# Performance work log

Hardware: AMD Instinct MI355X
Metric: run time of the kernel (lower is better)

## Reference

```python
import jax, jax.numpy as jnp
import numpy as np

N = 50000   # nodes
E = 800000  # edges (avg degree 16)
D = 128     # input feature dim
H = 128     # hidden dim
C = 10      # num classes
G = 16      # graphs in batch


def setup_inputs() -> dict:
    key = jax.random.key(0)
    ks = jax.random.split(key, 12)
    def w(k, shape):
        return jax.random.normal(k, shape, jnp.float32) / np.sqrt(shape[0]).astype(np.float32)
    return {
        "h": jax.random.normal(ks[0], (N, D), jnp.float32),
        "src": jax.random.randint(ks[1], (E,), 0, N, jnp.int32),
        "dst": jax.random.randint(ks[2], (E,), 0, N, jnp.int32),
        "graph_ids": jnp.sort(jax.random.randint(ks[3], (N,), 0, G, jnp.int32)),
        "W1a": w(ks[4], (D, H)), "b1a": jnp.zeros((H,), jnp.float32),
        "W2a": w(ks[5], (H, H)), "b2a": jnp.zeros((H,), jnp.float32),
        "W1b": w(ks[6], (H, H)), "b1b": jnp.zeros((H,), jnp.float32),
        "W2b": w(ks[7], (H, H)), "b2b": jnp.zeros((H,), jnp.float32),
        "Wc1": w(ks[8], (H, H)), "bc1": jnp.zeros((H,), jnp.float32),
        "Wc2": w(ks[9], (H, C)), "bc2": jnp.zeros((C,), jnp.float32),
    }


def _gin_layer(h, src, dst, W1, b1, W2, b2):
    # GIN aggregation, eps=0: z_i = h_i + sum_{j in N(i)} h_j
    agg = jax.ops.segment_sum(h[src], dst, num_segments=N)
    z = h + agg
    # 2-layer MLP apply function with relu activation ('relu' arg of GINLayer)
    z = jax.nn.relu(z @ W1 + b1)
    return jax.nn.relu(z @ W2 + b2)


def reference(h, src, dst, graph_ids, W1a, b1a, W2a, b2a,
              W1b, b1b, W2b, b2b, Wc1, bc1, Wc2, bc2):
    h = _gin_layer(h, src, dst, W1a, b1a, W2a, b2a)   # [N, H]
    h = _gin_layer(h, src, dst, W1b, b1b, W2b, b2b)   # [N, H]
    # dgl.mean_nodes over the batched graph
    sums = jax.ops.segment_sum(h, graph_ids, num_segments=G)                # [G, H]
    cnts = jax.ops.segment_sum(jnp.ones((N, 1), h.dtype), graph_ids, num_segments=G)
    h_g = sums / jnp.maximum(cnts, 1.0)
    # cls MLP: linear -> relu -> linear (logits)
    out = jax.nn.relu(h_g @ Wc1 + bc1) @ Wc2 + bc2    # [G, C]
    return out
```

## Files before the change

### kernel.cpp

```cpp
#include <hip/hip_runtime.h>
#include <stdint.h>

#define NN 50000
#define EE 800000
#define DD 128
#define GG 16
#define CC 10
#define NBK 196
#define BCH 4096
#define SMAX 5120
#define FT (NBK * NBK)
#define NSCN ((FT + 255) / 256)

typedef unsigned short u16;
typedef __bf16 bf16x8 __attribute__((ext_vector_type(8)));
typedef float f32x4 __attribute__((ext_vector_type(4)));
typedef unsigned int u32x4 __attribute__((ext_vector_type(4)));
typedef float fl4 __attribute__((ext_vector_type(4)));

__device__ inline u16 f2bf(float f) {
    unsigned u = __float_as_uint(f);
    u = u + 0x7fffu + ((u >> 16) & 1u);
    return (u16)(u >> 16);
}
__device__ inline unsigned pack2(float a, float b) {
    return (unsigned)f2bf(a) | ((unsigned)f2bf(b) << 16);
}
__device__ inline float bf2f(unsigned bits16) { return __uint_as_float(bits16 << 16); }
__device__ inline void acc8(float* a, uint4 v) {
    a[0] += __uint_as_float(v.x << 16); a[1] += __uint_as_float(v.x & 0xffff0000u);
    a[2] += __uint_as_float(v.y << 16); a[3] += __uint_as_float(v.y & 0xffff0000u);
    a[4] += __uint_as_float(v.z << 16); a[5] += __uint_as_float(v.z & 0xffff0000u);
    a[6] += __uint_as_float(v.w << 16); a[7] += __uint_as_float(v.w & 0xffff0000u);
}
__device__ inline void mand(uint4& v, int p) {
    unsigned m = p ? 0xffffffffu : 0u;
    v.x &= m; v.y &= m; v.z &= m; v.w &= m;
}
__device__ inline void nt_store16(void* p, uint4 v) {
    u32x4 x; x.x = v.x; x.y = v.y; x.z = v.z; x.w = v.w;
    __builtin_nontemporal_store(x, (u32x4*)p);
}
__device__ inline uint4 nt_load16(const void* p) {
    u32x4 x = __builtin_nontemporal_load((const u32x4*)p);
    uint4 r; r.x = x.x; r.y = x.y; r.z = x.z; r.w = x.w;
    return r;
}
__device__ inline float4 nt_loadf4(const float* p) {
    fl4 x = __builtin_nontemporal_load((const fl4*)p);
    float4 r; r.x = x.x; r.y = x.y; r.z = x.z; r.w = x.w;
    return r;
}

#define PZ (GG * DD)
#define PC (NN * DD / 4)
#define PW (4 * DD * DD)
#define PTOT (PZ + PC + PW)
#define PBLK ((PTOT + 255) / 256)

__global__ __launch_bounds__(256) void prepsort_kernel(
    const float* __restrict__ h,
    const float* __restrict__ a, const float* __restrict__ b,
    const float* __restrict__ c, const float* __restrict__ d,
    int* __restrict__ zbase, u16* __restrict__ H0, u16* __restrict__ wt,
    const int* __restrict__ dst, int* __restrict__ counts) {
    __shared__ int hist[NBK];
    int blk = blockIdx.x, t = threadIdx.x;
    if (blk < NBK) {
        for (int i = t; i < NBK; i += 256) hist[i] = 0;
        __syncthreads();
        int e0 = blk * BCH, e1 = min(e0 + BCH, EE);
        for (int e = e0 + t; e < e1; e += 256) atomicAdd(&hist[dst[e] >> 8], 1);
        __syncthreads();
        for (int i = t; i < NBK; i += 256) counts[i * NBK + blk] = hist[i];
        return;
    }
    int i = (blk - NBK) * 256 + t;
    if (i < PZ) { zbase[i] = 0; return; }
    i -= PZ;
    if (i < PC) {
        int j = i * 4;
        float4 v = nt_loadf4(h + j);
        ushort4 o;
        o.x = f2bf(v.x); o.y = f2bf(v.y); o.z = f2bf(v.z); o.w = f2bf(v.w);
        *(ushort4*)(H0 + j) = o;
        return;
    }
    i -= PC;
    if (i < PW) {
        int m = i >> 14, r = i & 16383, k = r >> 7, j = r & 127;
        const float* W = (m == 0) ? a : (m == 1) ? b : (m == 2) ? c : d;
        wt[(m << 14) + (j << 7) + k] = f2bf(W[(k << 7) + j]);
    }
}

__global__ __launch_bounds__(256) void scanA_kernel(int* __restrict__ counts,
                                                    int* __restrict__ bsum) {
    __shared__ int tmp[256];
    int t = threadIdx.x, idx = blockIdx.x * 256 + t;
    int v = (idx < FT) ? counts[idx] : 0;
    tmp[t] = v; __syncthreads();
    for (int off = 1; off < 256; off <<= 1) {
        int x = (t >= off) ? tmp[t - off] : 0;
        __syncthreads();
        tmp[t] += x;
        __syncthreads();
    }
    if (idx < FT) counts[idx] = tmp[t] - v;
    if (t == 255) bsum[blockIdx.x] = tmp[255];
}

__global__ __launch_bounds__(256) void scanB_kernel(int* __restrict__ bsum,
                                                    const int* __restrict__ gids,
                                                    int* __restrict__ gstart) {
    __shared__ int tmp[256];
    int t = threadIdx.x;
    if (t <= GG) {
        int lo = 0, hi = NN;
        while (lo < hi) { int mid = (lo + hi) >> 1; if (gids[mid] < t) lo = mid + 1; else hi = mid; }
        gstart[t] = lo;
    }
    int v = (t < NSCN) ? bsum[t] : 0;
    tmp[t] = v; __syncthreads();
    for (int off = 1; off < 256; off <<= 1) {
        int x = (t >= off) ? tmp[t - off] : 0;
        __syncthreads();
        tmp[t] += x;
        __syncthreads();
    }
    if (t < NSCN) bsum[t] = tmp[t] - v;
}

__global__ __launch_bounds__(256) void scanC_kernel(int* __restrict__ counts,
                                                    const int* __restrict__ bsum) {
    int idx = blockIdx.x * 256 + threadIdx.x;
    if (idx < FT) counts[idx] += bsum[blockIdx.x];
}

__global__ __launch_bounds__(256) void sortP3_kernel(const int* __restrict__ src,
                                                     const int* __restrict__ dst,
                                                     const int* __restrict__ counts,
                                                     int* __restrict__ epack) {
    __shared__ int lhist[NBK + 1];
    __shared__ int lcur[NBK];
    __shared__ int goff[NBK];
    __shared__ int tmp[256];
    __shared__ int sbuf[BCH];
    int b = blockIdx.x, t = threadIdx.x;
    int e0 = b * BCH, e1 = min(e0 + BCH, EE), n = e1 - e0;

    for (int i = t; i < NBK; i += 256) lhist[i] = 0;
    __syncthreads();
    for (int e = e0 + t; e < e1; e += 256) atomicAdd(&lhist[dst[e] >> 8], 1);
    __syncthreads();
    int v = (t < NBK) ? lhist[t] : 0;
    tmp[t] = v; __syncthreads();
    for (int off = 1; off < 256; off <<= 1) {
        int x = (t >= off) ? tmp[t - off] : 0;
        __syncthreads();
        tmp[t] += x;
        __syncthreads();
    }
    if (t < NBK) {
        int excl = tmp[t] - v;
        lcur[t] = excl;
        lhist[t] = excl;
        goff[t] = counts[t * NBK + b] - excl;
    }
    if (t == 0) lhist[NBK] = n;
    __syncthreads();
    for (int e = e0 + t; e < e1; e += 256) {
        int dd = dst[e], s = src[e];
        int p = atomicAdd(&lcur[dd >> 8], 1);
        sbuf[p] = (s << 8) | (dd & 255);
    }
    __syncthreads();
    for (int i = t; i < n; i += 256) {
        int pk = sbuf[i];
        int lo = 0, hi = NBK - 1;
        while (lo < hi) { int mid = (lo + hi + 1) >> 1; if (lhist[mid] <= i) lo = mid; else hi = mid - 1; }
        epack[goff[lo] + i] = pk;
    }
}

__global__ __launch_bounds__(256) void sortP4_kernel(const int* __restrict__ epack,
                                                     const int* __restrict__ counts,
                                                     int* __restrict__ offs,
                                                     int* __restrict__ ssrc) {
    __shared__ int hist[256];
    __shared__ int curs[256];
    __shared__ int stage[SMAX];
    int j = blockIdx.x, t = threadIdx.x;
    int n0 = j << 8;
    int b0 = counts[j * NBK];
    int b1 = (j < NBK - 1) ? counts[(j + 1) * NBK] : EE;
    hist[t] = 0;
    __syncthreads();
    for (int e = b0 + t; e < b1; e += 256) atomicAdd(&hist[epack[e] & 255], 1);
    __syncthreads();
    int deg = hist[t];
    for (int off = 1; off < 256; off <<= 1) {
        int x = (t >= off) ? hist[t - off] : 0;
        __syncthreads();
        hist[t] += x;
        __syncthreads();
    }
    int loff = hist[t] - deg;
    curs[t] = loff;
    if (n0 + t <= NN) offs[n0 + t] = b0 + loff;
    __syncthreads();
    for (int e = b0 + t; e < b1; e += 256) {
        int pk = epack[e];
        int p = atomicAdd(&curs[pk & 255], 1);
        stage[p] = pk >> 8;
    }
    __syncthreads();
    int n = b1 - b0;
    for (int i = t; i < n; i += 256) ssrc[b0 + i] = stage[i];
}

__global__ __launch_bounds__(256) void agg_kernel(
    const u16* __restrict__ Hin, const int* __restrict__ offs,
    const int* __restrict__ ssrc, u16* __restrict__ Z) {
    int gid = blockIdx.x * 32 + (threadIdx.x >> 3);
    int lid = threadIdx.x & 7;
    if (gid >= 2 * NN) return;
    int node = gid >> 1;
    int foff = (gid & 1) * 64 + lid * 8;
    const u16* base = Hin + foff;

    float acc[8] = {0.f, 0.f, 0.f, 0.f, 0.f, 0.f, 0.f, 0.f};
    uint4 vs = *(const uint4*)(base + (size_t)node * DD);
    int e0 = offs[node], e1 = offs[node + 1];
    acc8(acc, vs);

    int nch = (e1 - e0 + 7) >> 3;
    if (nch > 0) {
        int elast = e1 - 1;
        int i0 = ssrc[e0];
        int i1 = ssrc[min(e0 + 1, elast)];
        int i2 = ssrc[min(e0 + 2, elast)];
        int i3 = ssrc[min(e0 + 3, elast)];
        int i4 = ssrc[min(e0 + 4, elast)];
        int i5 = ssrc[min(e0 + 5, elast)];
        int i6 = ssrc[min(e0 + 6, elast)];
        int i7 = ssrc[min(e0 + 7, elast)];
        int eb = e0;
        for (int c = 0; c < nch; c++) {
            int ebn = eb + 8;
            int n0 = i0, n1 = i1, n2 = i2, n3 = i3, n4 = i4, n5 = i5, n6 = i6, n7 = i7;
            if (c + 1 < nch) {
                n0 = ssrc[ebn];
                n1 = ssrc[min(ebn + 1, elast)];
                n2 = ssrc[min(ebn + 2, elast)];
                n3 = ssrc[min(ebn + 3, elast)];
                n4 = ssrc[min(ebn + 4, elast)];
                n5 = ssrc[min(ebn + 5, elast)];
                n6 = ssrc[min(ebn + 6, elast)];
                n7 = ssrc[min(ebn + 7, elast)];
            }
            uint4 v0 = *(const uint4*)(base + (size_t)i0 * DD);
            uint4 v1 = *(const uint4*)(base + (size_t)i1 * DD);
            uint4 v2 = *(const uint4*)(base + (size_t)i2 * DD);
            uint4 v3 = *(const uint4*)(base + (size_t)i3 * DD);
            uint4 v4 = *(const uint4*)(base + (size_t)i4 * DD);
            uint4 v5 = *(const uint4*)(base + (size_t)i5 * DD);
            uint4 v6 = *(const uint4*)(base + (size_t)i6 * DD);
            uint4 v7 = *(const uint4*)(base + (size_t)i7 * DD);
            mand(v1, eb + 1 < e1); mand(v2, eb + 2 < e1); mand(v3, eb + 3 < e1);
            mand(v4, eb + 4 < e1); mand(v5, eb + 5 < e1); mand(v6, eb + 6 < e1);
            mand(v7, eb + 7 < e1);
            acc8(acc, v0); acc8(acc, v1); acc8(acc, v2); acc8(acc, v3);
            acc8(acc, v4); acc8(acc, v5); acc8(acc, v6); acc8(acc, v7);
            i0 = n0; i1 = n1; i2 = n2; i3 = n3; i4 = n4; i5 = n5; i6 = n6; i7 = n7;
            eb = ebn;
        }
    }
    uint4 o;
    o.x = pack2(acc[0], acc[1]); o.y = pack2(acc[2], acc[3]);
    o.z = pack2(acc[4], acc[5]); o.w = pack2(acc[6], acc[7]);
    nt_store16(Z + (size_t)node * DD + foff, o);
}

__global__ __launch_bounds__(256) void mlp_kernel(
    const u16* __restrict__ Zin, const u16* __restrict__ Wt1, const float* __restrict__ b1,
    const u16* __restrict__ Wt2, const float* __restrict__ b2,
    u16* __restrict__ Hout, const int* __restrict__ gids, float* __restrict__ pool) {
    __shared__ u16 zb[64][136];
    __shared__ int garr[64];
    const int tid = threadIdx.x;
    const int wave = tid >> 6;
    const int lane = tid & 63;
    const int m16 = lane & 15;
    const int quad = lane >> 4;
    const int row0 = blockIdx.x * 64 + wave * 16;
    const int brow0 = blockIdx.x * 64;

    if (pool && tid < 64) garr[tid] = (brow0 + tid < NN) ? gids[brow0 + tid] : 0;

#pragma unroll
    for (int p = 0; p < 4; p++) {
        int idx = p * 64 + lane;
        int r = idx >> 4, ch = idx & 15;
        if (row0 + r < NN) {
            uint4 v = nt_load16(Zin + (size_t)(row0 + r) * DD + ch * 8);
            *(uint4*)&zb[wave * 16 + r][ch * 8] = v;
        }
    }

    bf16x8 afr[4];
#pragma unroll
    for (int kk = 0; kk < 4; kk++)
        afr[kk] = *(const bf16x8*)&zb[wave * 16 + m16][kk * 32 + quad * 8];
    f32x4 acc[8];
#pragma unroll
    for (int nt = 0; nt < 8; nt++) acc[nt] = (f32x4){0.f, 0.f, 0.f, 0.f};
#pragma unroll
    for (int kk = 0; kk < 4; kk++) {
#pragma unroll
        for (int nt = 0; nt < 8; nt++) {
            bf16x8 bfr = *(const bf16x8*)(Wt1 + ((nt * 16 + m16) << 7) + kk * 32 + quad * 8);
            acc[nt] = __builtin_amdgcn_mfma_f32_16x16x32_bf16(afr[kk], bfr, acc[nt], 0, 0, 0);
        }
    }
#pragma unroll
    for (int nt = 0; nt < 8; nt++) {
        int col = nt * 16 + m16;
        float bias = b1[col];
#pragma unroll
        for (int r = 0; r < 4; r++) {
            float yv = acc[nt][r] + bias;
            yv = yv > 0.f ? yv : 0.f;
            zb[wave * 16 + quad * 4 + r][col] = f2bf(yv);
        }
    }

#pragma unroll
    for (int kk = 0; kk < 4; kk++)
        afr[kk] = *(const bf16x8*)&zb[wave * 16 + m16][kk * 32 + quad * 8];
#pragma unroll
    for (int nt = 0; nt < 8; nt++) acc[nt] = (f32x4){0.f, 0.f, 0.f, 0.f};
#pragma unroll
    for (int kk = 0; kk < 4; kk++) {
#pragma unroll
        for (int nt = 0; nt < 8; nt++) {
            bf16x8 bfr = *(const bf16x8*)(Wt2 + ((nt * 16 + m16) << 7) + kk * 32 + quad * 8);
            acc[nt] = __builtin_amdgcn_mfma_f32_16x16x32_bf16(afr[kk], bfr, acc[nt], 0, 0, 0);
        }
    }
#pragma unroll
    for (int nt = 0; nt < 8; nt++) {
        int col = nt * 16 + m16;
        float bias = b2[col];
#pragma unroll
        for (int r = 0; r < 4; r++) {
            float ov = acc[nt][r] + bias;
            ov = ov > 0.f ? ov : 0.f;
            zb[wave * 16 + quad * 4 + r][col] = f2bf(ov);
        }
    }
#pragma unroll
    for (int p = 0; p < 4; p++) {
        int idx = p * 64 + lane;
        int r = idx >> 4, ch = idx & 15;
        if (row0 + r < NN)
            nt_store16(Hout + (size_t)(row0 + r) * DD + ch * 8, *(const uint4*)&zb[wave * 16 + r][ch * 8]);
    }

    if (pool) {
        __syncthreads();
        if (tid < DD) {
            int cur = garr[0];
            float s = 0.f;
            for (int r = 0; r < 64; r++) {
                if (brow0 + r >= NN) break;
                int g = garr[r];
                if (g != cur) { atomicAdd(&pool[cur * DD + tid], s); s = 0.f; cur = g; }
                s += bf2f((unsigned)zb[r][tid]);
            }
            atomicAdd(&pool[cur * DD + tid], s);
        }
    }
}

__global__ void cls_kernel(const float* __restrict__ pool, const int* __restrict__ gstart,
                           const float* __restrict__ Wc1, const float* __restrict__ bc1,
                           const float* __restrict__ Wc2, const float* __restrict__ bc2,
                           float* __restrict__ out) {
    __shared__ float hg[128];
    __shared__ float y1[128];
    int g = blockIdx.x;
    int t = threadIdx.x;
    int cnt = gstart[g + 1] - gstart[g];
    float inv = 1.f / (float)(cnt > 1 ? cnt : 1);
    hg[t] = pool[g * DD + t] * inv;
    __syncthreads();
    float a = bc1[t];
    for (int k = 0; k < DD; k++) a += hg[k] * Wc1[k * DD + t];
    y1[t] = a > 0.f ? a : 0.f;
    __syncthreads();
    if (t < CC) {
        float o = bc2[t];
        for (int k = 0; k < DD; k++) o += y1[k] * Wc2[k * CC + t];
        out[g * CC + t] = o;
    }
}

extern "C" void kernel_launch(void* const* d_in, const int* in_sizes, int n_in,
                              void* d_out, int out_size, void* d_ws, size_t ws_size,
                              hipStream_t stream) {
    const float* h    = (const float*)d_in[0];
    const int*   src  = (const int*)d_in[1];
    const int*   dst  = (const int*)d_in[2];
    const int*   gids = (const int*)d_in[3];
    const float* W1a  = (const float*)d_in[4];
    const float* b1a  = (const float*)d_in[5];
    const float* W2a  = (const float*)d_in[6];
    const float* b2a  = (const float*)d_in[7];
    const float* W1b  = (const float*)d_in[8];
    const float* b1b  = (const float*)d_in[9];
    const float* W2b  = (const float*)d_in[10];
    const float* b2b  = (const float*)d_in[11];
    const float* Wc1  = (const float*)d_in[12];
    const float* bc1  = (const float*)d_in[13];
    const float* Wc2  = (const float*)d_in[14];
    const float* bc2  = (const float*)d_in[15];
    float* out = (float*)d_out;

    char* ws = (char*)d_ws;
    u16*   H0     = (u16*)(ws);
    u16*   H1     = (u16*)(ws + 12800000);
    u16*   H2     = (u16*)(ws + 25600000);
    u16*   Wt     = (u16*)(ws + 38400000);
    float* pool   = (float*)(ws + 38531072);
    int*   offs   = (int*)(ws + 38539264);
    int*   ssrc   = (int*)(ws + 38739268);
    int*   gstart = (int*)(ws + 41939268);
    int*   counts = (int*)(ws + 41939336);
    int*   bsum   = (int*)(ws + 42093000);
    int*   epack  = (int*)(ws + 42093792);
    u16*   Z1     = H2;
    u16*   Z2     = H0;

    prepsort_kernel<<<dim3(NBK + PBLK), dim3(256), 0, stream>>>(
        h, W1a, W2a, W1b, W2b, (int*)pool, H0, Wt, dst, counts);
    scanA_kernel<<<dim3(NSCN), dim3(256), 0, stream>>>(counts, bsum);
    scanB_kernel<<<dim3(1), dim3(256), 0, stream>>>(bsum, gids, gstart);
    scanC_kernel<<<dim3(NSCN), dim3(256), 0, stream>>>(counts, bsum);
    sortP3_kernel<<<dim3(NBK), dim3(256), 0, stream>>>(src, dst, counts, epack);
    sortP4_kernel<<<dim3(NBK), dim3(256), 0, stream>>>(epack, counts, offs, ssrc);
    agg_kernel<<<dim3((2 * NN + 31) / 32), dim3(256), 0, stream>>>(H0, offs, ssrc, Z1);
    mlp_kernel<<<dim3((NN + 63) / 64), dim3(256), 0, stream>>>(Z1, Wt, b1a, Wt + 16384, b2a, H1, gids, nullptr);
    agg_kernel<<<dim3((2 * NN + 31) / 32), dim3(256), 0, stream>>>(H1, offs, ssrc, Z2);
    mlp_kernel<<<dim3((NN + 63) / 64), dim3(256), 0, stream>>>(Z2, Wt + 32768, b1b, Wt + 49152, b2b, H2, gids, pool);
    cls_kernel<<<dim3(GG), dim3(128), 0, stream>>>(pool, gstart, Wc1, bc1, Wc2, bc2, out);
}
```

Measured before the change: 280.2 us.

## Make MLP kernel persistent with LDS/register-resident weights and prefetched input tiles

The MLP kernel now launches 256 persistent blocks that loop over 64-row tiles. Each block loads W1 once into LDS in MFMA fragment order and keeps W2 and both biases in registers. The next tile's input fragments are read straight from global memory while the current tile computes. The pooled second-layer call no longer writes the unused H output, and pooling is done per wave with shuffled graph ids. This removes the repeated per-block weight fetches and the input staging, at the cost of heavy register pressure (occupancy is pinned to 1), more pooling atomics, and reads of padded rows past N.

Measured after the change: 252.3 us. 1.11x faster.

```diff
diff --git a/kernel.cpp b/kernel.cpp
--- a/kernel.cpp
+++ b/kernel.cpp
@@ -11,6 +11,7 @@
 #define SMAX 5120
 #define FT (NBK * NBK)
 #define NSCN ((FT + 255) / 256)
+#define NT 782
 
 typedef unsigned short u16;
 typedef __bf16 bf16x8 __attribute__((ext_vector_type(8)));
@@ -40,11 +41,6 @@
 __device__ inline void nt_store16(void* p, uint4 v) {
     u32x4 x; x.x = v.x; x.y = v.y; x.z = v.z; x.w = v.w;
     __builtin_nontemporal_store(x, (u32x4*)p);
-}
-__device__ inline uint4 nt_load16(const void* p) {
-    u32x4 x = __builtin_nontemporal_load((const u32x4*)p);
-    uint4 r; r.x = x.x; r.y = x.y; r.z = x.z; r.w = x.w;
-    return r;
 }
 __device__ inline float4 nt_loadf4(const float* p) {
     fl4 x = __builtin_nontemporal_load((const fl4*)p);
@@ -282,104 +278,128 @@
     nt_store16(Z + (size_t)node * DD + foff, o);
 }
 
-__global__ __launch_bounds__(256) void mlp_kernel(
+__global__ __launch_bounds__(256, 1) void mlp_kernel(
     const u16* __restrict__ Zin, const u16* __restrict__ Wt1, const float* __restrict__ b1,
     const u16* __restrict__ Wt2, const float* __restrict__ b2,
     u16* __restrict__ Hout, const int* __restrict__ gids, float* __restrict__ pool) {
-    __shared__ u16 zb[64][136];
-    __shared__ int garr[64];
+    __shared__ __align__(16) u16 w1f[16384];
+    __shared__ __align__(16) u16 yb[64][136];
     const int tid = threadIdx.x;
     const int wave = tid >> 6;
     const int lane = tid & 63;
     const int m16 = lane & 15;
     const int quad = lane >> 4;
-    const int row0 = blockIdx.x * 64 + wave * 16;
-    const int brow0 = blockIdx.x * 64;
-
-    if (pool && tid < 64) garr[tid] = (brow0 + tid < NN) ? gids[brow0 + tid] : 0;
-
-#pragma unroll
-    for (int p = 0; p < 4; p++) {
-        int idx = p * 64 + lane;
-        int r = idx >> 4, ch = idx & 15;
-        if (row0 + r < NN) {
-            uint4 v = nt_load16(Zin + (size_t)(row0 + r) * DD + ch * 8);
-            *(uint4*)&zb[wave * 16 + r][ch * 8] = v;
-        }
-    }
-
-    bf16x8 afr[4];
+
+    for (int cidx = tid; cidx < 2048; cidx += 256) {
+        int ln = cidx & 63, nt = (cidx >> 6) & 7, kk = cidx >> 9;
+        int gofs = ((nt * 16 + (ln & 15)) << 7) + kk * 32 + (ln >> 4) * 8;
+        *(uint4*)&w1f[cidx * 8] = *(const uint4*)(Wt1 + gofs);
+    }
+    bf16x8 w2r[4][8];
 #pragma unroll
     for (int kk = 0; kk < 4; kk++)
-        afr[kk] = *(const bf16x8*)&zb[wave * 16 + m16][kk * 32 + quad * 8];
-    f32x4 acc[8];
-#pragma unroll
-    for (int nt = 0; nt < 8; nt++) acc[nt] = (f32x4){0.f, 0.f, 0.f, 0.f};
-#pragma unroll
-    for (int kk = 0; kk < 4; kk++) {
+#pragma unroll
+        for (int nt = 0; nt < 8; nt++)
+            w2r[kk][nt] = *(const bf16x8*)(Wt2 + ((nt * 16 + m16) << 7) + kk * 32 + quad * 8);
+    float bias1[8], bias2[8];
+#pragma unroll
+    for (int nt = 0; nt < 8; nt++) {
+        bias1[nt] = b1[nt * 16 + m16];
+        bias2[nt] = b2[nt * 16 + m16];
+    }
+    __syncthreads();
+
+    int tile = blockIdx.x;
+    bf16x8 afr[4], afrN[4];
+    {
+        size_t row = (size_t)(tile * 64 + wave * 16 + m16);
+#pragma unroll
+        for (int kk = 0; kk < 4; kk++)
+            afr[kk] = *(const bf16x8*)(Zin + row * DD + kk * 32 + quad * 8);
+    }
+    for (; tile < NT; tile += 256) {
+        int nxt = tile + 256;
+        if (nxt < NT) {
+            size_t row = (size_t)(nxt * 64 + wave * 16 + m16);
+#pragma unroll
+            for (int kk = 0; kk < 4; kk++)
+                afrN[kk] = *(const bf16x8*)(Zin + row * DD + kk * 32 + quad * 8);
+        }
+        const int row0 = tile * 64 + wave * 16;
+
+        f32x4 acc[8];
+#pragma unroll
+        for (int nt = 0; nt < 8; nt++) acc[nt] = (f32x4){0.f, 0.f, 0.f, 0.f};
+#pragma unroll
+        for (int kk = 0; kk < 4; kk++) {
+#pragma unroll
+            for (int nt = 0; nt < 8; nt++) {
+                bf16x8 bfr = *(const bf16x8*)&w1f[(((kk * 8 + nt) * 64) + lane) * 8];
+                acc[nt] = __builtin_amdgcn_mfma_f32_16x16x32_bf16(afr[kk], bfr, acc[nt], 0, 0, 0);
+            }
+        }
 #pragma unroll
         for (int nt = 0; nt < 8; nt++) {
-            bf16x8 bfr = *(const bf16x8*)(Wt1 + ((nt * 16 + m16) << 7) + kk * 32 + quad * 8);
-            acc[nt] = __builtin_amdgcn_mfma_f32_16x16x32_bf16(afr[kk], bfr, acc[nt], 0, 0, 0);
-        }
-    }
-#pragma unroll
-    for (int nt = 0; nt < 8; nt++) {
-        int col = nt * 16 + m16;
-        float bias = b1[col];
-#pragma unroll
-        for (int r = 0; r < 4; r++) {
-            float yv = acc[nt][r] + bias;
-            yv = yv > 0.f ? yv : 0.f;
-            zb[wave * 16 + quad * 4 + r][col] = f2bf(yv);
-        }
-    }
-
-#pragma unroll
-    for (int kk = 0; kk < 4; kk++)
-        afr[kk] = *(const bf16x8*)&zb[wave * 16 + m16][kk * 32 + quad * 8];
-#pragma unroll
-    for (int nt = 0; nt < 8; nt++) acc[nt] = (f32x4){0.f, 0.f, 0.f, 0.f};
-#pragma unroll
-    for (int kk = 0; kk < 4; kk++) {
+            int col = nt * 16 + m16;
+#pragma unroll
+            for (int r = 0; r < 4; r++) {
+                float yv = acc[nt][r] + bias1[nt];
+                yv = yv > 0.f ? yv : 0.f;
+                yb[wave * 16 + quad * 4 + r][col] = f2bf(yv);
+            }
+        }
+
+        bf16x8 afr2[4];
+#pragma unroll
+        for (int kk = 0; kk < 4; kk++)
+            afr2[kk] = *(const bf16x8*)&yb[wave * 16 + m16][kk * 32 + quad * 8];
+#pragma unroll
+        for (int nt = 0; nt < 8; nt++) acc[nt] = (f32x4){0.f, 0.f, 0.f, 0.f};
+#pragma unroll
+        for (int kk = 0; kk < 4; kk++) {
+#pragma unroll
+            for (int nt = 0; nt < 8; nt++)
+                acc[nt] = __builtin_amdgcn_mfma_f32_16x16x32_bf16(afr2[kk], w2r[kk][nt], acc[nt], 0, 0, 0);
+        }
 #pragma unroll
         for (int nt = 0; nt < 8; nt++) {
-            bf16x8 bfr = *(const bf16x8*)(Wt2 + ((nt * 16 + m16) << 7) + kk * 32 + quad * 8);
-            acc[nt] = __builtin_amdgcn_mfma_f32_16x16x32_bf16(afr[kk], bfr, acc[nt], 0, 0, 0);
-        }
-    }
-#pragma unroll
-    for (int nt = 0; nt < 8; nt++) {
-        int col = nt * 16 + m16;
-        float bias = b2[col];
-#pragma unroll
-        for (int r = 0; r < 4; r++) {
-            float ov = acc[nt][r] + bias;
-            ov = ov > 0.f ? ov : 0.f;
-            zb[wave * 16 + quad * 4 + r][col] = f2bf(ov);
-        }
-    }
-#pragma unroll
-    for (int p = 0; p < 4; p++) {
-        int idx = p * 64 + lane;
-        int r = idx >> 4, ch = idx & 15;
-        if (row0 + r < NN)
-            nt_store16(Hout + (size_t)(row0 + r) * DD + ch * 8, *(const uint4*)&zb[wave * 16 + r][ch * 8]);
-    }
-
-    if (pool) {
-        __syncthreads();
-        if (tid < DD) {
-            int cur = garr[0];
-            float s = 0.f;
-            for (int r = 0; r < 64; r++) {
-                if (brow0 + r >= NN) break;
-                int g = garr[r];
-                if (g != cur) { atomicAdd(&pool[cur * DD + tid], s); s = 0.f; cur = g; }
-                s += bf2f((unsigned)zb[r][tid]);
-            }
-            atomicAdd(&pool[cur * DD + tid], s);
-        }
+            int col = nt * 16 + m16;
+#pragma unroll
+            for (int r = 0; r < 4; r++) {
+                float ov = acc[nt][r] + bias2[nt];
+                ov = ov > 0.f ? ov : 0.f;
+                yb[wave * 16 + quad * 4 + r][col] = f2bf(ov);
+            }
+        }
+        if (!pool) {
+#pragma unroll
+            for (int p = 0; p < 4; p++) {
+                int idx = p * 64 + lane;
+                int r = idx >> 4, ch = idx & 15;
+                if (row0 - wave * 16 + ((wave * 16) + r) < NN) {}
+                int grow = row0 + r;
+                if (grow < NN)
+                    *(uint4*)(Hout + (size_t)grow * DD + ch * 8) = *(const uint4*)&yb[wave * 16 + r][ch * 8];
+            }
+        } else {
+            int prow = row0 + m16;
+            int g = gids[min(prow, NN - 1)];
+#pragma unroll
+            for (int fsel = 0; fsel < 2; fsel++) {
+                int f = lane + fsel * 64;
+                float s = 0.f;
+                int cur = __shfl(g, 0);
+                for (int r = 0; r < 16; r++) {
+                    int gr = __shfl(g, r);
+                    float v = (row0 + r < NN) ? bf2f((unsigned)yb[wave * 16 + r][f]) : 0.f;
+                    if (gr != cur) { atomicAdd(&pool[cur * DD + f], s); s = 0.f; cur = gr; }
+                    s += v;
+                }
+                atomicAdd(&pool[cur * DD + f], s);
+            }
+        }
+#pragma unroll
+        for (int kk = 0; kk < 4; kk++) afr[kk] = afrN[kk];
     }
 }
 
@@ -450,8 +470,8 @@
     sortP3_kernel<<<dim3(NBK), dim3(256), 0, stream>>>(src, dst, counts, epack);
     sortP4_kernel<<<dim3(NBK), dim3(256), 0, stream>>>(epack, counts, offs, ssrc);
     agg_kernel<<<dim3((2 * NN + 31) / 32), dim3(256), 0, stream>>>(H0, offs, ssrc, Z1);
-    mlp_kernel<<<dim3((NN + 63) / 64), dim3(256), 0, stream>>>(Z1, Wt, b1a, Wt + 16384, b2a, H1, gids, nullptr);
+    mlp_kernel<<<dim3(256), dim3(256), 0, stream>>>(Z1, Wt, b1a, Wt + 16384, b2a, H1, gids, nullptr);
     agg_kernel<<<dim3((2 * NN + 31) / 32), dim3(256), 0, stream>>>(H1, offs, ssrc, Z2);
-    mlp_kernel<<<dim3((NN + 63) / 64), dim3(256), 0, stream>>>(Z2, Wt + 32768, b1b, Wt + 49152, b2b, H2, gids, pool);
+    mlp_kernel<<<dim3(256), dim3(256), 0, stream>>>(Z2, Wt + 32768, b1b, Wt + 49152, b2b, H2, gids, pool);
     cls_kernel<<<dim3(GG), dim3(128), 0, stream>>>(pool, gstart, Wc1, bc1, Wc2, bc2, out);
 }
```
